# Performance work log

Measured on AMD Instinct MI355X. Metric: run time of the kernel, lower is better.

The kernel has to match this reference:

```python
import jax, jax.numpy as jnp
import numpy as np

B, N, NPOINT, NSAMPLE = 8, 8192, 2048, 64
RADIUS = 0.2
C_IN = 64  # input feature channels; mlp[0]=64 -> 67 after use_xyz concat


def setup_inputs() -> dict:
    key = jax.random.key(0)
    ks = jax.random.split(key, 12)
    xyz = jax.random.uniform(ks[0], (B, N, 3), dtype=jnp.float32)
    features = jax.random.normal(ks[1], (B, N, C_IN), dtype=jnp.float32)
    inds = jax.random.randint(ks[2], (B, NPOINT), 0, N, dtype=jnp.int32)

    def mkw(k, cin, cout):
        return jax.random.normal(k, (cin, cout), jnp.float32) * (1.0 / np.sqrt(cin).astype(np.float32))

    w0 = mkw(ks[3], C_IN + 3, 64)
    w1 = mkw(ks[4], 64, 64)
    w2 = mkw(ks[5], 64, 128)
    # BN (inference) folded into per-channel scale/shift
    s0 = 1.0 + 0.1 * jax.random.normal(ks[6], (64,), jnp.float32)
    t0 = 0.1 * jax.random.normal(ks[7], (64,), jnp.float32)
    s1 = 1.0 + 0.1 * jax.random.normal(ks[8], (64,), jnp.float32)
    t1 = 0.1 * jax.random.normal(ks[9], (64,), jnp.float32)
    s2 = 1.0 + 0.1 * jax.random.normal(ks[10], (128,), jnp.float32)
    t2 = 0.1 * jax.random.normal(ks[11], (128,), jnp.float32)
    return dict(xyz=xyz, features=features, inds=inds,
                w0=w0, s0=s0, t0=t0, w1=w1, s1=s1, t1=t1, w2=w2, s2=s2, t2=t2)


def _ball_query(xyz, new_xyz):
    """First NSAMPLE point indices within RADIUS of each query; pad by repeating
    the first hit (matches CUDA ball_query semantics). xyz:(B,N,3) new_xyz:(B,S,3)."""
    nn = jnp.sum(xyz * xyz, axis=-1)            # (B,N)
    qq = jnp.sum(new_xyz * new_xyz, axis=-1)    # (B,S)
    d2 = qq[:, :, None] + nn[:, None, :] - 2.0 * jnp.einsum('bsc,bnc->bsn', new_xyz, xyz)
    within = d2 < (RADIUS * RADIUS)
    ar = jnp.arange(N, dtype=jnp.int32)
    keyed = jnp.where(within, ar[None, None, :], N)   # out-of-radius -> sentinel N
    keyed = jnp.sort(keyed, axis=-1)[:, :, :NSAMPLE]  # first hits in point order
    idx = jnp.where(keyed == N, keyed[:, :, :1], keyed)
    return jnp.minimum(idx, N - 1)


_gather = jax.vmap(lambda pts, i: pts[i])  # (N,C),(M,) -> (M,C) per batch


def reference(xyz, features, inds, w0, s0, t0, w1, s1, t1, w2, s2, t2):
    new_xyz = _gather(xyz, inds)                              # (B,S,3)
    idx = _ball_query(xyz, new_xyz)                           # (B,S,ns)
    flat = idx.reshape(B, NPOINT * NSAMPLE)
    g_xyz = _gather(xyz, flat).reshape(B, NPOINT, NSAMPLE, 3)
    g_xyz = (g_xyz - new_xyz[:, :, None, :]) / RADIUS         # normalize_xyz
    g_feat = _gather(features, flat).reshape(B, NPOINT, NSAMPLE, C_IN)
    x = jnp.concatenate([g_xyz, g_feat], axis=-1)             # (B,S,ns,C+3)
    for wgt, s, t in ((w0, s0, t0), (w1, s1, t1), (w2, s2, t2)):
        x = jax.nn.relu(jnp.einsum('bpsc,cd->bpsd', x, wgt) * s + t)
    new_features = jnp.max(x, axis=2)                         # max-pool over nsample
    return new_xyz, new_features, inds, idx
```

## Files before the change

kernel.cpp:

```cpp
#include <hip/hip_runtime.h>

#define BB 8
#define NN 8192
#define NPOINT 2048
#define NSAMPLE 64
#define CIN 64
#define RADIUS 0.2f
#define R2 (RADIUS * RADIUS)

#define OFF_NEWXYZ 0
#define OFF_FEAT (BB * NPOINT * 3)
#define OFF_INDS (OFF_FEAT + BB * NPOINT * 128)
#define OFF_IDX (OFF_INDS + BB * NPOINT)

typedef _Float16 half8 __attribute__((ext_vector_type(8)));
typedef _Float16 half4 __attribute__((ext_vector_type(4)));
typedef __fp16 f16x2 __attribute__((ext_vector_type(2)));
typedef float floatx16 __attribute__((ext_vector_type(16)));
typedef unsigned int uint2v __attribute__((ext_vector_type(2)));

#define P0 88
#define P1 72
#define X_LOC 0
#define H_LOC (64 * P0)
#define XH_WAVE (64 * P0 + 64 * P1)
#define WT0_S 0
#define WT1_S (64 * P0)
#define WT2_S (64 * P0 + 64 * P1)

#define QPW_FB 8
#define QPW_G 2

#define WSF16H (BB * NN * CIN)
#define WT0_OFF WSF16H
#define WT1_OFF (WT0_OFF + 64 * 80)
#define WT2_OFF (WT1_OFF + 64 * 64)
#define WS_END (WT2_OFF + 128 * 64)
#define WS_NEED ((size_t)WS_END * 2)

__global__ __launch_bounds__(256) void ballq_kernel(
    const float* __restrict__ xyz, const int* __restrict__ inds,
    float* __restrict__ out, const float* __restrict__ features,
    _Float16* __restrict__ ws16, const float* __restrict__ w0,
    const float* __restrict__ s0, const float* __restrict__ t0,
    const float* __restrict__ w1, const float* __restrict__ s1,
    const float* __restrict__ w2, const float* __restrict__ s2) {
  if (ws16) {
    const int t = blockIdx.x * 256 + threadIdx.x;
    const float4* src = (const float4*)features;
    const float4 a = src[2 * t + 0];
    const float4 b = src[2 * t + 1];
    union {
      half8 v;
      f16x2 p[4];
    } u;
    u.p[0] = __builtin_amdgcn_cvt_pkrtz(a.x, a.y);
    u.p[1] = __builtin_amdgcn_cvt_pkrtz(a.z, a.w);
    u.p[2] = __builtin_amdgcn_cvt_pkrtz(b.x, b.y);
    u.p[3] = __builtin_amdgcn_cvt_pkrtz(b.z, b.w);
    ((half8*)ws16)[t] = u.v;
    if (blockIdx.x == 0) {
      const int tt = threadIdx.x;
      if (tt < 64) {
        const int d = tt;
        const float sd = s0[d], td = t0[d];
        _Float16* row = ws16 + WT0_OFF + d * 80;
        for (int c = 0; c < 80; ++c) {
          float v = 0.0f;
          if (c < 64) v = w0[(3 + c) * 64 + d] * sd;
          else if (c < 67) v = w0[(c - 64) * 64 + d] * sd;
          else if (c == 67) v = td;
          row[c] = (_Float16)v;
        }
      } else if (tt < 128) {
        const int d = tt - 64;
        const float sd = s1[d];
        _Float16* row = ws16 + WT1_OFF + d * 64;
        for (int c = 0; c < 64; ++c) row[c] = (_Float16)(w1[c * 64 + d] * sd);
      } else {
        const int d2 = tt - 128;
        const float sd = s2[d2];
        _Float16* row = ws16 + WT2_OFF + d2 * 64;
        for (int c = 0; c < 64; ++c) row[c] = (_Float16)(w2[c * 128 + d2] * sd);
      }
    }
  }

  __shared__ int sidx[4][2][NSAMPLE];
  const int wave = (blockIdx.x * 256 + threadIdx.x) >> 6;
  const int lane = threadIdx.x & 63;
  const int wid = threadIdx.x >> 6;
  const int q0 = wave * 2, q1 = q0 + 1;
  const int b = q0 >> 11;

  const float* xb = xyz + (size_t)b * NN * 3;
  const int i0 = inds[q0], i1 = inds[q1];
  const float c0x = xb[i0 * 3 + 0], c0y = xb[i0 * 3 + 1], c0z = xb[i0 * 3 + 2];
  const float c1x = xb[i1 * 3 + 0], c1y = xb[i1 * 3 + 1], c1z = xb[i1 * 3 + 2];

  if (lane < 2) {
    const int qq_ = lane ? q1 : q0;
    const int ii = lane ? i1 : i0;
    out[OFF_NEWXYZ + (size_t)qq_ * 3 + 0] = lane ? c1x : c0x;
    out[OFF_NEWXYZ + (size_t)qq_ * 3 + 1] = lane ? c1y : c0y;
    out[OFF_NEWXYZ + (size_t)qq_ * 3 + 2] = lane ? c1z : c0z;
    out[OFF_INDS + qq_] = (float)ii;
  }

  const float qq0 = c0x * c0x + c0y * c0y + c0z * c0z;
  const float qq1 = c1x * c1x + c1y * c1y + c1z * c1z;

  int cnt0 = 0, cnt1 = 0;
  float ax[4], ay[4], az[4];
#pragma unroll
  for (int k = 0; k < 4; ++k) {
    const float* p = xb + (size_t)(k * 64 + lane) * 3;
    ax[k] = p[0];
    ay[k] = p[1];
    az[k] = p[2];
  }
  for (int j0 = 0; j0 < NN; j0 += 256) {
    float bx[4] = {0}, by[4] = {0}, bz[4] = {0};
    const int jn = j0 + 256;
    if (jn < NN) {
#pragma unroll
      for (int k = 0; k < 4; ++k) {
        const float* p = xb + (size_t)(jn + k * 64 + lane) * 3;
        bx[k] = p[0];
        by[k] = p[1];
        bz[k] = p[2];
      }
    }
#pragma unroll
    for (int k = 0; k < 4; ++k) {
      const int j = j0 + k * 64 + lane;
      const float nn_ = ax[k] * ax[k] + ay[k] * ay[k] + az[k] * az[k];
      const float dot0 = c0x * ax[k] + c0y * ay[k] + c0z * az[k];
      const float dot1 = c1x * ax[k] + c1y * ay[k] + c1z * az[k];
      const bool hit0 = (qq0 + nn_ - 2.0f * dot0) < R2;
      const bool hit1 = (qq1 + nn_ - 2.0f * dot1) < R2;
      const unsigned long long m0 = __ballot(hit0);
      const unsigned long long m1 = __ballot(hit1);
      if (hit0) {
        const int pos = cnt0 + (int)__popcll(m0 & ((1ull << lane) - 1ull));
        if (pos < NSAMPLE) sidx[wid][0][pos] = j;
      }
      if (hit1) {
        const int pos = cnt1 + (int)__popcll(m1 & ((1ull << lane) - 1ull));
        if (pos < NSAMPLE) sidx[wid][1][pos] = j;
      }
      cnt0 += (int)__popcll(m0);
      cnt1 += (int)__popcll(m1);
    }
    if (cnt0 >= NSAMPLE && cnt1 >= NSAMPLE) break;
#pragma unroll
    for (int k = 0; k < 4; ++k) {
      ax[k] = bx[k];
      ay[k] = by[k];
      az[k] = bz[k];
    }
  }
  const int v0 = sidx[wid][0][lane < cnt0 ? lane : 0];
  out[OFF_IDX + (size_t)q0 * NSAMPLE + lane] = (float)v0;
  const int v1 = sidx[wid][1][lane < cnt1 ? lane : 0];
  out[OFF_IDX + (size_t)q1 * NSAMPLE + lane] = (float)v1;
}

__device__ inline unsigned int pkru(float a, float b) {
  union {
    f16x2 p;
    unsigned int u;
  } t;
  t.p = __builtin_amdgcn_cvt_pkrtz(fmaxf(a, 0.0f), fmaxf(b, 0.0f));
  return t.u;
}
__device__ inline void build_frags(const floatx16& acc, half8& f0, half8& f1) {
  unsigned int P[4], Q[4];
#pragma unroll
  for (int rg = 0; rg < 4; ++rg) {
    P[rg] = pkru(acc[4 * rg + 0], acc[4 * rg + 1]);
    Q[rg] = pkru(acc[4 * rg + 2], acc[4 * rg + 3]);
  }
  union {
    unsigned int u[4];
    half8 h;
  } o;
  uint2v sp = __builtin_amdgcn_permlane32_swap(P[0], P[1], false, false);
  uint2v sq = __builtin_amdgcn_permlane32_swap(Q[0], Q[1], false, false);
  o.u[0] = sp.x; o.u[1] = sq.x; o.u[2] = sp.y; o.u[3] = sq.y;
  f0 = o.h;
  sp = __builtin_amdgcn_permlane32_swap(P[2], P[3], false, false);
  sq = __builtin_amdgcn_permlane32_swap(Q[2], Q[3], false, false);
  o.u[0] = sp.x; o.u[1] = sq.x; o.u[2] = sp.y; o.u[3] = sq.y;
  f1 = o.h;
}

__global__ __launch_bounds__(64) void mlp_g(
    const float* __restrict__ xyz, const _Float16* __restrict__ ws16,
    const int* __restrict__ inds, const float* __restrict__ t1,
    const float* __restrict__ t2, float* __restrict__ out) {
  __shared__ _Float16 sm[64 * P0];
  const int l = threadIdx.x & 63;
  const int l31 = l & 31;
  const int h5 = l >> 5;
  const int koff = h5 * 8;

  _Float16* xbuf = sm;
  {
    half8 z = {};
    *(half8*)&xbuf[l * P0 + 72] = z;
  }

  const int lb = (blockIdx.x & 7) * ((int)gridDim.x >> 3) + (blockIdx.x >> 3);
  const int wq0 = lb * QPW_G;
  const int b = wq0 >> 11;
  const float* xb = xyz + (size_t)b * NN * 3;
  const _Float16* fb16 = ws16 + (size_t)b * NN * CIN;

  float t2v[4];
#pragma unroll
  for (int ct = 0; ct < 4; ++ct) t2v[ct] = t2[ct * 32 + l31];
  float t1f[2][16];
#pragma unroll
  for (int nt = 0; nt < 2; ++nt)
#pragma unroll
    for (int rg = 0; rg < 4; ++rg) {
      const float4 tq = *(const float4*)(t1 + nt * 32 + 8 * rg + 4 * h5);
      t1f[nt][4 * rg + 0] = tq.x;
      t1f[nt][4 * rg + 1] = tq.y;
      t1f[nt][4 * rg + 2] = tq.z;
      t1f[nt][4 * rg + 3] = tq.w;
    }

  int myidx = (int)out[OFF_IDX + (size_t)wq0 * NSAMPLE + l];
  int indv = inds[wq0];
  float cx = xb[indv * 3 + 0], cy = xb[indv * 3 + 1], cz = xb[indv * 3 + 2];
  float ppx = xb[myidx * 3 + 0], ppy = xb[myidx * 3 + 1],
        ppz = xb[myidx * 3 + 2];

  unsigned long long wbu = (unsigned long long)(ws16 + WT0_OFF);

#pragma unroll 1
  for (int qi = 0; qi < QPW_G; ++qi) {
    const int q = wq0 + qi;
    const int nq = (qi + 1 < QPW_G) ? q + 1 : q;
    asm volatile("" : "+s"(wbu));
    const _Float16* wt0 = (const _Float16*)wbu;
    const _Float16* wt1q = wt0 + 64 * 80;
    const _Float16* wt2q = wt0 + 64 * 80 + 64 * 64;

    half8 gh[8];
#pragma unroll
    for (int i = 0; i < 8; ++i) {
      const int r = (l >> 3) + 8 * i;
      const int sidx = __shfl(myidx, r, 64);
      gh[i] = *(const half8*)(fb16 + (size_t)sidx * CIN + (l & 7) * 8);
    }
    half8 b0w[2][5];
#pragma unroll
    for (int nt = 0; nt < 2; ++nt)
#pragma unroll
      for (int ks = 0; ks < 5; ++ks)
        b0w[nt][ks] =
            *(const half8*)&wt0[(nt * 32 + l31) * 80 + ks * 16 + koff];
    const float fni = out[OFF_IDX + (size_t)nq * NSAMPLE + l];
    const int nindv = inds[nq];

#pragma unroll
    for (int i = 0; i < 8; ++i) {
      const int r = (l >> 3) + 8 * i;
      *(half8*)&xbuf[r * P0 + (l & 7) * 8] = gh[i];
    }
    {
      union {
        half8 v;
        f16x2 p[4];
      } xv;
      xv.p[0] =
          __builtin_amdgcn_cvt_pkrtz((ppx - cx) * 5.0f, (ppy - cy) * 5.0f);
      xv.p[1] = __builtin_amdgcn_cvt_pkrtz((ppz - cz) * 5.0f, 1.0f);
      xv.p[2] = __builtin_amdgcn_cvt_pkrtz(0.0f, 0.0f);
      xv.p[3] = __builtin_amdgcn_cvt_pkrtz(0.0f, 0.0f);
      *(half8*)&xbuf[l * P0 + 64] = xv.v;
    }

    half8 xa1[2][4];
    {
      half8 xa[2][5];
#pragma unroll
      for (int st = 0; st < 2; ++st)
#pragma unroll
        for (int ks = 0; ks < 5; ++ks)
          xa[st][ks] =
              *(const half8*)&xbuf[(st * 32 + l31) * P0 + ks * 16 + koff];
#pragma unroll
      for (int nt = 0; nt < 2; ++nt)
#pragma unroll
        for (int st = 0; st < 2; ++st) {
          floatx16 acc;
#pragma unroll
          for (int i = 0; i < 16; ++i) acc[i] = 0.0f;
#pragma unroll
          for (int ks = 0; ks < 5; ++ks)
            acc = __builtin_amdgcn_mfma_f32_32x32x16_f16(b0w[nt][ks],
                                                         xa[st][ks], acc,
                                                         0, 0, 0);
          build_frags(acc, xa1[st][2 * nt], xa1[st][2 * nt + 1]);
        }
    }

    const int nidxs = (int)fni;
    const float ncx = xb[nindv * 3 + 0];
    const float ncy = xb[nindv * 3 + 1];
    const float ncz = xb[nindv * 3 + 2];
    const float nppx = xb[nidxs * 3 + 0];
    const float nppy = xb[nidxs * 3 + 1];
    const float nppz = xb[nidxs * 3 + 2];

    half8 h1a[2][4];
    {
      half8 b1w[2][4];
#pragma unroll
      for (int nt = 0; nt < 2; ++nt)
#pragma unroll
        for (int ks = 0; ks < 4; ++ks)
          b1w[nt][ks] =
              *(const half8*)&wt1q[(nt * 32 + l31) * 64 + ks * 16 + koff];
#pragma unroll
      for (int nt = 0; nt < 2; ++nt)
#pragma unroll
        for (int st = 0; st < 2; ++st) {
          floatx16 acc;
#pragma unroll
          for (int i = 0; i < 16; ++i) acc[i] = t1f[nt][i];
#pragma unroll
          for (int ks = 0; ks < 4; ++ks)
            acc = __builtin_amdgcn_mfma_f32_32x32x16_f16(b1w[nt][ks],
                                                         xa1[st][ks], acc,
                                                         0, 0, 0);
          build_frags(acc, h1a[st][2 * nt], h1a[st][2 * nt + 1]);
        }
    }

    {
      half8 b2c[4], b2n[4];
#pragma unroll
      for (int ks = 0; ks < 4; ++ks)
        b2c[ks] = *(const half8*)&wt2q[l31 * 64 + ks * 16 + koff];
#pragma unroll
      for (int ct = 0; ct < 4; ++ct) {
        if (ct < 3) {
#pragma unroll
          for (int ks = 0; ks < 4; ++ks)
            b2n[ks] = *(const half8*)&wt2q[((ct + 1) * 32 + l31) * 64 +
                                           ks * 16 + koff];
        }
        floatx16 aA, aB;
#pragma unroll
        for (int i = 0; i < 16; ++i) {
          aA[i] = 0.0f;
          aB[i] = 0.0f;
        }
#pragma unroll
        for (int ks = 0; ks < 4; ++ks) {
          aA = __builtin_amdgcn_mfma_f32_32x32x16_f16(h1a[0][ks], b2c[ks],
                                                      aA, 0, 0, 0);
          aB = __builtin_amdgcn_mfma_f32_32x32x16_f16(h1a[1][ks], b2c[ks],
                                                      aB, 0, 0, 0);
        }
        float m = fmaxf(aA[0], aB[0]);
#pragma unroll
        for (int i = 1; i < 16; ++i) m = fmaxf(m, fmaxf(aA[i], aB[i]));
        float v = fmaxf(m + t2v[ct], 0.0f);
        v = fmaxf(v, __shfl_xor(v, 32, 64));
        if (l < 32) out[OFF_FEAT + (size_t)q * 128 + ct * 32 + l] = v;
#pragma unroll
        for (int ks = 0; ks < 4; ++ks) b2c[ks] = b2n[ks];
      }
    }

    myidx = nidxs;
    cx = ncx; cy = ncy; cz = ncz;
    ppx = nppx; ppy = nppy; ppz = nppz;
  }
}

__global__ __launch_bounds__(128, 2) void mlp_fb(
    const float* __restrict__ xyz, const float* __restrict__ features,
    const int* __restrict__ inds,
    const float* __restrict__ w0, const float* __restrict__ s0,
    const float* __restrict__ t0, const float* __restrict__ w1,
    const float* __restrict__ s1, const float* __restrict__ t1,
    const float* __restrict__ w2, const float* __restrict__ s2,
    const float* __restrict__ t2, float* __restrict__ out) {
  __shared__ _Float16 sm[2 * XH_WAVE];
  const int tid = threadIdx.x;
  const int w = tid >> 6;
  const int l = tid & 63;
  const int l31 = l & 31;
  const int h5 = l >> 5;
  const int koff = h5 * 8;

  {
    const int d = tid >> 1, hf = tid & 1;
    const float sd0 = s0[d], td0 = t0[d], sd1 = s1[d];
#pragma unroll
    for (int j = 0; j < 44; ++j) {
      const int c = hf * 44 + j;
      float v = 0.0f;
      if (c < 64) v = w0[(3 + c) * 64 + d] * sd0;
      else if (c < 67) v = w0[(c - 64) * 64 + d] * sd0;
      else if (c == 67) v = td0;
      sm[WT0_S + d * P0 + c] = (_Float16)v;
    }
#pragma unroll
    for (int j = 0; j < 32; ++j) {
      const int c = hf * 32 + j;
      sm[WT1_S + d * P1 + c] = (_Float16)(w1[c * 64 + d] * sd1);
    }
    const int ch = tid;
    const float sch = s2[ch];
#pragma unroll
    for (int c = 0; c < 64; ++c)
      sm[WT2_S + ch * P1 + c] = (_Float16)(w2[c * 128 + ch] * sch);
  }
  __syncthreads();

  half8 b0f[2][5], b1f[2][4], b2f[4][4];
#pragma unroll
  for (int nt = 0; nt < 2; ++nt)
#pragma unroll
    for (int ks = 0; ks < 5; ++ks)
      b0f[nt][ks] =
          *(const half8*)&sm[WT0_S + (nt * 32 + l31) * P0 + ks * 16 + koff];
#pragma unroll
  for (int nt = 0; nt < 2; ++nt)
#pragma unroll
    for (int ks = 0; ks < 4; ++ks)
      b1f[nt][ks] =
          *(const half8*)&sm[WT1_S + (nt * 32 + l31) * P1 + ks * 16 + koff];
#pragma unroll
  for (int ct = 0; ct < 4; ++ct)
#pragma unroll
    for (int ks = 0; ks < 4; ++ks)
      b2f[ct][ks] =
          *(const half8*)&sm[WT2_S + (ct * 32 + l31) * P1 + ks * 16 + koff];
  const float t1v0 = t1[l31];
  const float t1v1 = t1[32 + l31];
  float t2v[4];
#pragma unroll
  for (int ct = 0; ct < 4; ++ct) t2v[ct] = t2[ct * 32 + l31];
  __syncthreads();

  _Float16* xbuf = sm + w * XH_WAVE + X_LOC;
  _Float16* hbuf = sm + w * XH_WAVE + H_LOC;
  {
    half8 z = {};
    *(half8*)&xbuf[l * P0 + 72] = z;
  }

  const int lb = (blockIdx.x & 7) * ((int)gridDim.x >> 3) + (blockIdx.x >> 3);
  const int wq0 = (lb * 2 + w) * QPW_FB;
  const int b = wq0 >> 11;
  const float* xb = xyz + (size_t)b * NN * 3;
  const float* fbase = features + (size_t)b * NN * CIN;

  int myidx = (int)out[OFF_IDX + (size_t)wq0 * NSAMPLE + l];
  int indv = inds[wq0];
  float cx = xb[indv * 3 + 0], cy = xb[indv * 3 + 1], cz = xb[indv * 3 + 2];
  float ppx = xb[myidx * 3 + 0], ppy = xb[myidx * 3 + 1],
        ppz = xb[myidx * 3 + 2];

#pragma unroll 1
  for (int qi = 0; qi < QPW_FB; ++qi) {
    const int q = wq0 + qi;
    const int nq = (qi + 1 < QPW_FB) ? q + 1 : q;

    float4 g[16];
#pragma unroll
    for (int i = 0; i < 16; ++i) {
      const int s = (l >> 2) + 16 * (i & 3);
      const int c = (l & 3) + 4 * (i >> 2);
      const int sidx = __shfl(myidx, s, 64);
      g[i] = *(const float4*)(fbase + (size_t)sidx * CIN + 4 * c);
    }
    const float fni = out[OFF_IDX + (size_t)nq * NSAMPLE + l];
    const int nindv = inds[nq];

#pragma unroll
    for (int i = 0; i < 16; ++i) {
      const int s = (l >> 2) + 16 * (i & 3);
      const int c = (l & 3) + 4 * (i >> 2);
      union {
        half4 v;
        f16x2 p[2];
      } hv;
      hv.p[0] = __builtin_amdgcn_cvt_pkrtz(g[i].x, g[i].y);
      hv.p[1] = __builtin_amdgcn_cvt_pkrtz(g[i].z, g[i].w);
      *(half4*)&xbuf[s * P0 + 4 * c] = hv.v;
    }
    {
      union {
        half8 v;
        f16x2 p[4];
      } xv;
      xv.p[0] =
          __builtin_amdgcn_cvt_pkrtz((ppx - cx) * 5.0f, (ppy - cy) * 5.0f);
      xv.p[1] = __builtin_amdgcn_cvt_pkrtz((ppz - cz) * 5.0f, 1.0f);
      xv.p[2] = __builtin_amdgcn_cvt_pkrtz(0.0f, 0.0f);
      xv.p[3] = __builtin_amdgcn_cvt_pkrtz(0.0f, 0.0f);
      *(half8*)&xbuf[l * P0 + 64] = xv.v;
    }

    {
      half8 xa[2][5];
#pragma unroll
      for (int st = 0; st < 2; ++st)
#pragma unroll
        for (int ks = 0; ks < 5; ++ks)
          xa[st][ks] =
              *(const half8*)&xbuf[(st * 32 + l31) * P0 + ks * 16 + koff];
#pragma unroll
      for (int nt = 0; nt < 2; ++nt)
#pragma unroll
        for (int st = 0; st < 2; ++st) {
          floatx16 acc;
#pragma unroll
          for (int i = 0; i < 16; ++i) acc[i] = 0.0f;
#pragma unroll
          for (int ks = 0; ks < 5; ++ks)
            acc = __builtin_amdgcn_mfma_f32_32x32x16_f16(xa[st][ks],
                                                         b0f[nt][ks], acc,
                                                         0, 0, 0);
#pragma unroll
          for (int reg = 0; reg < 16; ++reg) {
            const int row = st * 32 + (reg & 3) + 8 * (reg >> 2) + 4 * h5;
            hbuf[row * P1 + nt * 32 + l31] = (_Float16)fmaxf(acc[reg], 0.0f);
          }
        }
    }

    const int nidxs = (int)fni;
    const float ncx = xb[nindv * 3 + 0];
    const float ncy = xb[nindv * 3 + 1];
    const float ncz = xb[nindv * 3 + 2];
    const float nppx = xb[nidxs * 3 + 0];
    const float nppy = xb[nidxs * 3 + 1];
    const float nppz = xb[nidxs * 3 + 2];

    {
      half8 ha[2][4];
#pragma unroll
      for (int st = 0; st < 2; ++st)
#pragma unroll
        for (int ks = 0; ks < 4; ++ks)
          ha[st][ks] =
              *(const half8*)&hbuf[(st * 32 + l31) * P1 + ks * 16 + koff];
#pragma unroll
      for (int nt = 0; nt < 2; ++nt) {
        const float tt = nt ? t1v1 : t1v0;
#pragma unroll
        for (int st = 0; st < 2; ++st) {
          floatx16 acc;
#pragma unroll
          for (int i = 0; i < 16; ++i) acc[i] = 0.0f;
#pragma unroll
          for (int ks = 0; ks < 4; ++ks)
            acc = __builtin_amdgcn_mfma_f32_32x32x16_f16(ha[st][ks],
                                                         b1f[nt][ks], acc,
                                                         0, 0, 0);
#pragma unroll
          for (int reg = 0; reg < 16; ++reg) {
            const int row = st * 32 + (reg & 3) + 8 * (reg >> 2) + 4 * h5;
            xbuf[row * P0 + nt * 32 + l31] =
                (_Float16)fmaxf(acc[reg] + tt, 0.0f);
          }
        }
      }
    }

    {
      half8 h1a[2][4];
#pragma unroll
      for (int st = 0; st < 2; ++st)
#pragma unroll
        for (int ks = 0; ks < 4; ++ks)
          h1a[st][ks] =
              *(const half8*)&xbuf[(st * 32 + l31) * P0 + ks * 16 + koff];
#pragma unroll
      for (int ct = 0; ct < 4; ++ct) {
        floatx16 aA, aB;
#pragma unroll
        for (int i = 0; i < 16; ++i) {
          aA[i] = 0.0f;
          aB[i] = 0.0f;
        }
#pragma unroll
        for (int ks = 0; ks < 4; ++ks) {
          aA = __builtin_amdgcn_mfma_f32_32x32x16_f16(h1a[0][ks], b2f[ct][ks],
                                                      aA, 0, 0, 0);
          aB = __builtin_amdgcn_mfma_f32_32x32x16_f16(h1a[1][ks], b2f[ct][ks],
                                                      aB, 0, 0, 0);
        }
        float m = fmaxf(aA[0], aB[0]);
#pragma unroll
        for (int i = 1; i < 16; ++i) m = fmaxf(m, fmaxf(aA[i], aB[i]));
        float v = fmaxf(m + t2v[ct], 0.0f);
        v = fmaxf(v, __shfl_xor(v, 32, 64));
        if (l < 32) out[OFF_FEAT + (size_t)q * 128 + ct * 32 + l] = v;
      }
    }

    myidx = nidxs;
    cx = ncx; cy = ncy; cz = ncz;
    ppx = nppx; ppy = nppy; ppz = nppz;
  }
}

extern "C" void kernel_launch(void* const* d_in, const int* in_sizes, int n_in,
                              void* d_out, int out_size, void* d_ws,
                              size_t ws_size, hipStream_t stream) {
  const float* xyz = (const float*)d_in[0];
  const float* features = (const float*)d_in[1];
  const int* inds = (const int*)d_in[2];
  const float* w0 = (const float*)d_in[3];
  const float* s0 = (const float*)d_in[4];
  const float* t0 = (const float*)d_in[5];
  const float* w1 = (const float*)d_in[6];
  const float* s1 = (const float*)d_in[7];
  const float* t1 = (const float*)d_in[8];
  const float* w2 = (const float*)d_in[9];
  const float* s2 = (const float*)d_in[10];
  const float* t2 = (const float*)d_in[11];
  float* out = (float*)d_out;

  _Float16* ws16 = (ws_size >= WS_NEED) ? (_Float16*)d_ws : nullptr;

  const int nquery = BB * NPOINT;
  ballq_kernel<<<nquery / 8, 256, 0, stream>>>(xyz, inds, out, features, ws16,
                                               w0, s0, t0, w1, s1, w2, s2);
  if (ws16) {
    mlp_g<<<nquery / QPW_G, 64, 0, stream>>>(xyz, ws16, inds, t1, t2, out);
  } else {
    mlp_fb<<<nquery / (2 * QPW_FB), 128, 0, stream>>>(
        xyz, features, inds, w0, s0, t0, w1, s1, t1, w2, s2, t2, out);
  }
}
```

Measured before the change: 183.2 us.

## Fuse ball query into MLP kernel and split fp16 prep into separate kernel

The ball-query search now runs inside the per-wave MLP kernel, so each wave finds its two queries' neighbour indices in LDS and feeds them straight into the MFMA MLP. This avoids the global round-trip of neighbour indices and the separate ball-query launch. Feature and weight fp16 conversion moves to its own prep kernel. The trade-off is that the MLP kernel runs a long serial search per 64-thread block, and the prep kernel becomes a separate launch ahead of it.

```diff
diff --git a/kernel.cpp b/kernel.cpp
--- a/kernel.cpp
+++ b/kernel.cpp
@@ -29,7 +29,6 @@
 #define WT2_S (64 * P0 + 64 * P1)
 
 #define QPW_FB 8
-#define QPW_G 2
 
 #define WSF16H (BB * NN * CIN)
 #define WT0_OFF WSF16H
@@ -38,132 +37,50 @@
 #define WS_END (WT2_OFF + 128 * 64)
 #define WS_NEED ((size_t)WS_END * 2)
 
-__global__ __launch_bounds__(256) void ballq_kernel(
-    const float* __restrict__ xyz, const int* __restrict__ inds,
-    float* __restrict__ out, const float* __restrict__ features,
-    _Float16* __restrict__ ws16, const float* __restrict__ w0,
-    const float* __restrict__ s0, const float* __restrict__ t0,
-    const float* __restrict__ w1, const float* __restrict__ s1,
-    const float* __restrict__ w2, const float* __restrict__ s2) {
-  if (ws16) {
-    const int t = blockIdx.x * 256 + threadIdx.x;
-    const float4* src = (const float4*)features;
-    const float4 a = src[2 * t + 0];
-    const float4 b = src[2 * t + 1];
-    union {
-      half8 v;
-      f16x2 p[4];
-    } u;
-    u.p[0] = __builtin_amdgcn_cvt_pkrtz(a.x, a.y);
-    u.p[1] = __builtin_amdgcn_cvt_pkrtz(a.z, a.w);
-    u.p[2] = __builtin_amdgcn_cvt_pkrtz(b.x, b.y);
-    u.p[3] = __builtin_amdgcn_cvt_pkrtz(b.z, b.w);
-    ((half8*)ws16)[t] = u.v;
-    if (blockIdx.x == 0) {
-      const int tt = threadIdx.x;
-      if (tt < 64) {
-        const int d = tt;
-        const float sd = s0[d], td = t0[d];
-        _Float16* row = ws16 + WT0_OFF + d * 80;
-        for (int c = 0; c < 80; ++c) {
-          float v = 0.0f;
-          if (c < 64) v = w0[(3 + c) * 64 + d] * sd;
-          else if (c < 67) v = w0[(c - 64) * 64 + d] * sd;
-          else if (c == 67) v = td;
-          row[c] = (_Float16)v;
-        }
-      } else if (tt < 128) {
-        const int d = tt - 64;
-        const float sd = s1[d];
-        _Float16* row = ws16 + WT1_OFF + d * 64;
-        for (int c = 0; c < 64; ++c) row[c] = (_Float16)(w1[c * 64 + d] * sd);
-      } else {
-        const int d2 = tt - 128;
-        const float sd = s2[d2];
-        _Float16* row = ws16 + WT2_OFF + d2 * 64;
-        for (int c = 0; c < 64; ++c) row[c] = (_Float16)(w2[c * 128 + d2] * sd);
-      }
-    }
-  }
-
-  __shared__ int sidx[4][2][NSAMPLE];
-  const int wave = (blockIdx.x * 256 + threadIdx.x) >> 6;
-  const int lane = threadIdx.x & 63;
-  const int wid = threadIdx.x >> 6;
-  const int q0 = wave * 2, q1 = q0 + 1;
-  const int b = q0 >> 11;
-
-  const float* xb = xyz + (size_t)b * NN * 3;
-  const int i0 = inds[q0], i1 = inds[q1];
-  const float c0x = xb[i0 * 3 + 0], c0y = xb[i0 * 3 + 1], c0z = xb[i0 * 3 + 2];
-  const float c1x = xb[i1 * 3 + 0], c1y = xb[i1 * 3 + 1], c1z = xb[i1 * 3 + 2];
-
-  if (lane < 2) {
-    const int qq_ = lane ? q1 : q0;
-    const int ii = lane ? i1 : i0;
-    out[OFF_NEWXYZ + (size_t)qq_ * 3 + 0] = lane ? c1x : c0x;
-    out[OFF_NEWXYZ + (size_t)qq_ * 3 + 1] = lane ? c1y : c0y;
-    out[OFF_NEWXYZ + (size_t)qq_ * 3 + 2] = lane ? c1z : c0z;
-    out[OFF_INDS + qq_] = (float)ii;
-  }
-
-  const float qq0 = c0x * c0x + c0y * c0y + c0z * c0z;
-  const float qq1 = c1x * c1x + c1y * c1y + c1z * c1z;
-
-  int cnt0 = 0, cnt1 = 0;
-  float ax[4], ay[4], az[4];
-#pragma unroll
-  for (int k = 0; k < 4; ++k) {
-    const float* p = xb + (size_t)(k * 64 + lane) * 3;
-    ax[k] = p[0];
-    ay[k] = p[1];
-    az[k] = p[2];
-  }
-  for (int j0 = 0; j0 < NN; j0 += 256) {
-    float bx[4] = {0}, by[4] = {0}, bz[4] = {0};
-    const int jn = j0 + 256;
-    if (jn < NN) {
-#pragma unroll
-      for (int k = 0; k < 4; ++k) {
-        const float* p = xb + (size_t)(jn + k * 64 + lane) * 3;
-        bx[k] = p[0];
-        by[k] = p[1];
-        bz[k] = p[2];
-      }
-    }
-#pragma unroll
-    for (int k = 0; k < 4; ++k) {
-      const int j = j0 + k * 64 + lane;
-      const float nn_ = ax[k] * ax[k] + ay[k] * ay[k] + az[k] * az[k];
-      const float dot0 = c0x * ax[k] + c0y * ay[k] + c0z * az[k];
-      const float dot1 = c1x * ax[k] + c1y * ay[k] + c1z * az[k];
-      const bool hit0 = (qq0 + nn_ - 2.0f * dot0) < R2;
-      const bool hit1 = (qq1 + nn_ - 2.0f * dot1) < R2;
-      const unsigned long long m0 = __ballot(hit0);
-      const unsigned long long m1 = __ballot(hit1);
-      if (hit0) {
-        const int pos = cnt0 + (int)__popcll(m0 & ((1ull << lane) - 1ull));
-        if (pos < NSAMPLE) sidx[wid][0][pos] = j;
-      }
-      if (hit1) {
-        const int pos = cnt1 + (int)__popcll(m1 & ((1ull << lane) - 1ull));
-        if (pos < NSAMPLE) sidx[wid][1][pos] = j;
-      }
-      cnt0 += (int)__popcll(m0);
-      cnt1 += (int)__popcll(m1);
-    }
-    if (cnt0 >= NSAMPLE && cnt1 >= NSAMPLE) break;
-#pragma unroll
-    for (int k = 0; k < 4; ++k) {
-      ax[k] = bx[k];
-      ay[k] = by[k];
-      az[k] = bz[k];
-    }
-  }
-  const int v0 = sidx[wid][0][lane < cnt0 ? lane : 0];
-  out[OFF_IDX + (size_t)q0 * NSAMPLE + lane] = (float)v0;
-  const int v1 = sidx[wid][1][lane < cnt1 ? lane : 0];
-  out[OFF_IDX + (size_t)q1 * NSAMPLE + lane] = (float)v1;
+__global__ __launch_bounds__(256) void prep_kernel(
+    const float* __restrict__ features, _Float16* __restrict__ ws16,
+    const float* __restrict__ w0, const float* __restrict__ s0,
+    const float* __restrict__ t0, const float* __restrict__ w1,
+    const float* __restrict__ s1, const float* __restrict__ w2,
+    const float* __restrict__ s2) {
+  const int t = blockIdx.x * 256 + threadIdx.x;
+  const float4* src = (const float4*)features;
+  const float4 a = src[2 * t + 0];
+  const float4 b = src[2 * t + 1];
+  union {
+    half8 v;
+    f16x2 p[4];
+  } u;
+  u.p[0] = __builtin_amdgcn_cvt_pkrtz(a.x, a.y);
+  u.p[1] = __builtin_amdgcn_cvt_pkrtz(a.z, a.w);
+  u.p[2] = __builtin_amdgcn_cvt_pkrtz(b.x, b.y);
+  u.p[3] = __builtin_amdgcn_cvt_pkrtz(b.z, b.w);
+  ((half8*)ws16)[t] = u.v;
+  if (blockIdx.x == 0) {
+    const int tt = threadIdx.x;
+    if (tt < 64) {
+      const int d = tt;
+      const float sd = s0[d], td = t0[d];
+      _Float16* row = ws16 + WT0_OFF + d * 80;
+      for (int c = 0; c < 80; ++c) {
+        float v = 0.0f;
+        if (c < 64) v = w0[(3 + c) * 64 + d] * sd;
+        else if (c < 67) v = w0[(c - 64) * 64 + d] * sd;
+        else if (c == 67) v = td;
+        row[c] = (_Float16)v;
+      }
+    } else if (tt < 128) {
+      const int d = tt - 64;
+      const float sd = s1[d];
+      _Float16* row = ws16 + WT1_OFF + d * 64;
+      for (int c = 0; c < 64; ++c) row[c] = (_Float16)(w1[c * 64 + d] * sd);
+    } else {
+      const int d2 = tt - 128;
+      const float sd = s2[d2];
+      _Float16* row = ws16 + WT2_OFF + d2 * 64;
+      for (int c = 0; c < 64; ++c) row[c] = (_Float16)(w2[c * 128 + d2] * sd);
+    }
+  }
 }
 
 __device__ inline unsigned int pkru(float a, float b) {
@@ -195,7 +112,7 @@
   f1 = o.h;
 }
 
-__global__ __launch_bounds__(64) void mlp_g(
+__global__ __launch_bounds__(64) void fused_g(
     const float* __restrict__ xyz, const _Float16* __restrict__ ws16,
     const int* __restrict__ inds, const float* __restrict__ t1,
     const float* __restrict__ t2, float* __restrict__ out) {
@@ -205,17 +122,88 @@
   const int h5 = l >> 5;
   const int koff = h5 * 8;
 
-  _Float16* xbuf = sm;
-  {
-    half8 z = {};
-    *(half8*)&xbuf[l * P0 + 72] = z;
-  }
-
   const int lb = (blockIdx.x & 7) * ((int)gridDim.x >> 3) + (blockIdx.x >> 3);
-  const int wq0 = lb * QPW_G;
-  const int b = wq0 >> 11;
+  const int q0 = lb * 2, q1 = q0 + 1;
+  const int b = q0 >> 11;
   const float* xb = xyz + (size_t)b * NN * 3;
   const _Float16* fb16 = ws16 + (size_t)b * NN * CIN;
+
+  int* sidxL = (int*)sm;
+  const int i0 = inds[q0], i1 = inds[q1];
+  const float c0x = xb[i0 * 3 + 0], c0y = xb[i0 * 3 + 1], c0z = xb[i0 * 3 + 2];
+  const float c1x = xb[i1 * 3 + 0], c1y = xb[i1 * 3 + 1], c1z = xb[i1 * 3 + 2];
+
+  if (l < 2) {
+    const int qq_ = l ? q1 : q0;
+    const int ii = l ? i1 : i0;
+    out[OFF_NEWXYZ + (size_t)qq_ * 3 + 0] = l ? c1x : c0x;
+    out[OFF_NEWXYZ + (size_t)qq_ * 3 + 1] = l ? c1y : c0y;
+    out[OFF_NEWXYZ + (size_t)qq_ * 3 + 2] = l ? c1z : c0z;
+    out[OFF_INDS + qq_] = (float)ii;
+  }
+
+  const float qq0 = c0x * c0x + c0y * c0y + c0z * c0z;
+  const float qq1 = c1x * c1x + c1y * c1y + c1z * c1z;
+
+  int cnt0 = 0, cnt1 = 0;
+  float ax[4], ay[4], az[4];
+#pragma unroll
+  for (int k = 0; k < 4; ++k) {
+    const float* p = xb + (size_t)(k * 64 + l) * 3;
+    ax[k] = p[0];
+    ay[k] = p[1];
+    az[k] = p[2];
+  }
+  for (int j0 = 0; j0 < NN; j0 += 256) {
+    float bx[4] = {0}, by[4] = {0}, bz[4] = {0};
+    const int jn = j0 + 256;
+    if (jn < NN) {
+#pragma unroll
+      for (int k = 0; k < 4; ++k) {
+        const float* p = xb + (size_t)(jn + k * 64 + l) * 3;
+        bx[k] = p[0];
+        by[k] = p[1];
+        bz[k] = p[2];
+      }
+    }
+#pragma unroll
+    for (int k = 0; k < 4; ++k) {
+      const int j = j0 + k * 64 + l;
+      const float nn_ = ax[k] * ax[k] + ay[k] * ay[k] + az[k] * az[k];
+      const float dot0 = c0x * ax[k] + c0y * ay[k] + c0z * az[k];
+      const float dot1 = c1x * ax[k] + c1y * ay[k] + c1z * az[k];
+      const bool hit0 = (qq0 + nn_ - 2.0f * dot0) < R2;
+      const bool hit1 = (qq1 + nn_ - 2.0f * dot1) < R2;
+      const unsigned long long m0 = __ballot(hit0);
+      const unsigned long long m1 = __ballot(hit1);
+      if (hit0) {
+        const int pos = cnt0 + (int)__popcll(m0 & ((1ull << l) - 1ull));
+        if (pos < NSAMPLE) sidxL[pos] = j;
+      }
+      if (hit1) {
+        const int pos = cnt1 + (int)__popcll(m1 & ((1ull << l) - 1ull));
+        if (pos < NSAMPLE) sidxL[64 + pos] = j;
+      }
+      cnt0 += (int)__popcll(m0);
+      cnt1 += (int)__popcll(m1);
+    }
+    if (cnt0 >= NSAMPLE && cnt1 >= NSAMPLE) break;
+#pragma unroll
+    for (int k = 0; k < 4; ++k) {
+      ax[k] = bx[k];
+      ay[k] = by[k];
+      az[k] = bz[k];
+    }
+  }
+  const int v0 = sidxL[l < cnt0 ? l : 0];
+  out[OFF_IDX + (size_t)q0 * NSAMPLE + l] = (float)v0;
+  const int v1 = sidxL[64 + (l < cnt1 ? l : 0)];
+  out[OFF_IDX + (size_t)q1 * NSAMPLE + l] = (float)v1;
+
+  const float pp0x = xb[v0 * 3 + 0], pp0y = xb[v0 * 3 + 1],
+              pp0z = xb[v0 * 3 + 2];
+  const float pp1x = xb[v1 * 3 + 0], pp1y = xb[v1 * 3 + 1],
+              pp1z = xb[v1 * 3 + 2];
 
   float t2v[4];
 #pragma unroll
@@ -232,18 +220,20 @@
       t1f[nt][4 * rg + 3] = tq.w;
     }
 
-  int myidx = (int)out[OFF_IDX + (size_t)wq0 * NSAMPLE + l];
-  int indv = inds[wq0];
-  float cx = xb[indv * 3 + 0], cy = xb[indv * 3 + 1], cz = xb[indv * 3 + 2];
-  float ppx = xb[myidx * 3 + 0], ppy = xb[myidx * 3 + 1],
-        ppz = xb[myidx * 3 + 2];
+  _Float16* xbuf = sm;
+  {
+    half8 z = {};
+    *(half8*)&xbuf[l * P0 + 72] = z;
+  }
 
   unsigned long long wbu = (unsigned long long)(ws16 + WT0_OFF);
+  int myidx = v0;
+  float cx = c0x, cy = c0y, cz = c0z;
+  float ppx = pp0x, ppy = pp0y, ppz = pp0z;
 
 #pragma unroll 1
-  for (int qi = 0; qi < QPW_G; ++qi) {
-    const int q = wq0 + qi;
-    const int nq = (qi + 1 < QPW_G) ? q + 1 : q;
+  for (int qi = 0; qi < 2; ++qi) {
+    const int q = q0 + qi;
     asm volatile("" : "+s"(wbu));
     const _Float16* wt0 = (const _Float16*)wbu;
     const _Float16* wt1q = wt0 + 64 * 80;
@@ -263,8 +253,6 @@
       for (int ks = 0; ks < 5; ++ks)
         b0w[nt][ks] =
             *(const half8*)&wt0[(nt * 32 + l31) * 80 + ks * 16 + koff];
-    const float fni = out[OFF_IDX + (size_t)nq * NSAMPLE + l];
-    const int nindv = inds[nq];
 
 #pragma unroll
     for (int i = 0; i < 8; ++i) {
@@ -309,14 +297,6 @@
         }
     }
 
-    const int nidxs = (int)fni;
-    const float ncx = xb[nindv * 3 + 0];
-    const float ncy = xb[nindv * 3 + 1];
-    const float ncz = xb[nindv * 3 + 2];
-    const float nppx = xb[nidxs * 3 + 0];
-    const float nppy = xb[nidxs * 3 + 1];
-    const float nppz = xb[nidxs * 3 + 2];
-
     half8 h1a[2][4];
     {
       half8 b1w[2][4];
@@ -379,10 +359,93 @@
       }
     }
 
-    myidx = nidxs;
-    cx = ncx; cy = ncy; cz = ncz;
-    ppx = nppx; ppy = nppy; ppz = nppz;
-  }
+    myidx = v1;
+    cx = c1x; cy = c1y; cz = c1z;
+    ppx = pp1x; ppy = pp1y; ppz = pp1z;
+  }
+}
+
+__global__ __launch_bounds__(256) void ballq_kernel(
+    const float* __restrict__ xyz, const int* __restrict__ inds,
+    float* __restrict__ out) {
+  __shared__ int sidx[4][2][NSAMPLE];
+  const int wave = (blockIdx.x * 256 + threadIdx.x) >> 6;
+  const int lane = threadIdx.x & 63;
+  const int wid = threadIdx.x >> 6;
+  const int q0 = wave * 2, q1 = q0 + 1;
+  const int b = q0 >> 11;
+
+  const float* xb = xyz + (size_t)b * NN * 3;
+  const int i0 = inds[q0], i1 = inds[q1];
+  const float c0x = xb[i0 * 3 + 0], c0y = xb[i0 * 3 + 1], c0z = xb[i0 * 3 + 2];
+  const float c1x = xb[i1 * 3 + 0], c1y = xb[i1 * 3 + 1], c1z = xb[i1 * 3 + 2];
+
+  if (lane < 2) {
+    const int qq_ = lane ? q1 : q0;
+    const int ii = lane ? i1 : i0;
+    out[OFF_NEWXYZ + (size_t)qq_ * 3 + 0] = lane ? c1x : c0x;
+    out[OFF_NEWXYZ + (size_t)qq_ * 3 + 1] = lane ? c1y : c0y;
+    out[OFF_NEWXYZ + (size_t)qq_ * 3 + 2] = lane ? c1z : c0z;
+    out[OFF_INDS + qq_] = (float)ii;
+  }
+
+  const float qq0 = c0x * c0x + c0y * c0y + c0z * c0z;
+  const float qq1 = c1x * c1x + c1y * c1y + c1z * c1z;
+
+  int cnt0 = 0, cnt1 = 0;
+  float ax[4], ay[4], az[4];
+#pragma unroll
+  for (int k = 0; k < 4; ++k) {
+    const float* p = xb + (size_t)(k * 64 + lane) * 3;
+    ax[k] = p[0];
+    ay[k] = p[1];
+    az[k] = p[2];
+  }
+  for (int j0 = 0; j0 < NN; j0 += 256) {
+    float bx[4] = {0}, by[4] = {0}, bz[4] = {0};
+    const int jn = j0 + 256;
+    if (jn < NN) {
+#pragma unroll
+      for (int k = 0; k < 4; ++k) {
+        const float* p = xb + (size_t)(jn + k * 64 + lane) * 3;
+        bx[k] = p[0];
+        by[k] = p[1];
+        bz[k] = p[2];
+      }
+    }
+#pragma unroll
+    for (int k = 0; k < 4; ++k) {
+      const int j = j0 + k * 64 + lane;
+      const float nn_ = ax[k] * ax[k] + ay[k] * ay[k] + az[k] * az[k];
+      const float dot0 = c0x * ax[k] + c0y * ay[k] + c0z * az[k];
+      const float dot1 = c1x * ax[k] + c1y * ay[k] + c1z * az[k];
+      const bool hit0 = (qq0 + nn_ - 2.0f * dot0) < R2;
+      const bool hit1 = (qq1 + nn_ - 2.0f * dot1) < R2;
+      const unsigned long long m0 = __ballot(hit0);
+      const unsigned long long m1 = __ballot(hit1);
+      if (hit0) {
+        const int pos = cnt0 + (int)__popcll(m0 & ((1ull << lane) - 1ull));
+        if (pos < NSAMPLE) sidx[wid][0][pos] = j;
+      }
+      if (hit1) {
+        const int pos = cnt1 + (int)__popcll(m1 & ((1ull << lane) - 1ull));
+        if (pos < NSAMPLE) sidx[wid][1][pos] = j;
+      }
+      cnt0 += (int)__popcll(m0);
+      cnt1 += (int)__popcll(m1);
+    }
+    if (cnt0 >= NSAMPLE && cnt1 >= NSAMPLE) break;
+#pragma unroll
+    for (int k = 0; k < 4; ++k) {
+      ax[k] = bx[k];
+      ay[k] = by[k];
+      az[k] = bz[k];
+    }
+  }
+  const int v0 = sidx[wid][0][lane < cnt0 ? lane : 0];
+  out[OFF_IDX + (size_t)q0 * NSAMPLE + lane] = (float)v0;
+  const int v1 = sidx[wid][1][lane < cnt1 ? lane : 0];
+  out[OFF_IDX + (size_t)q1 * NSAMPLE + lane] = (float)v1;
 }
 
 __global__ __launch_bounds__(128, 2) void mlp_fb(
@@ -637,11 +700,12 @@
   _Float16* ws16 = (ws_size >= WS_NEED) ? (_Float16*)d_ws : nullptr;
 
   const int nquery = BB * NPOINT;
-  ballq_kernel<<<nquery / 8, 256, 0, stream>>>(xyz, inds, out, features, ws16,
-                                               w0, s0, t0, w1, s1, w2, s2);
   if (ws16) {
-    mlp_g<<<nquery / QPW_G, 64, 0, stream>>>(xyz, ws16, inds, t1, t2, out);
+    prep_kernel<<<2048, 256, 0, stream>>>(features, ws16, w0, s0, t0, w1, s1,
+                                          w2, s2);
+    fused_g<<<nquery / 2, 64, 0, stream>>>(xyz, ws16, inds, t1, t2, out);
   } else {
+    ballq_kernel<<<nquery / 8, 256, 0, stream>>>(xyz, inds, out);
     mlp_fb<<<nquery / (2 * QPW_FB), 128, 0, stream>>>(
         xyz, features, inds, w0, s0, t0, w1, s1, t1, w2, s2, t2, out);
   }
```

After: 209.3 us. +14.2%, slower.
